# Performance work log

Hardware: AMD Instinct MI355X
Metric: run time of the kernel (lower is better)

Reference implementation:

```python
import jax, jax.numpy as jnp
import numpy as np

N_NODES = 100000
HIDDEN = 128
N_EDGES = 640000


def setup_inputs() -> dict:
    key = jax.random.key(0)
    k1, k2, k3, k4 = jax.random.split(key, 4)
    z_state = jax.random.normal(k1, (N_NODES, HIDDEN), dtype=jnp.float32)
    edge_label_index = jax.random.randint(k2, (2, N_EDGES), 0, N_NODES, dtype=jnp.int64)
    # Kaiming-ish init scale for the two linear layers (torch default ~ U(-1/sqrt(fan_in), ...))
    w1 = jax.random.normal(k3, (2 * HIDDEN, HIDDEN), dtype=jnp.float32) * (1.0 / np.sqrt(2 * HIDDEN))
    b1 = jnp.zeros((HIDDEN,), dtype=jnp.float32)
    w2 = jax.random.normal(k4, (HIDDEN, 1), dtype=jnp.float32) * (1.0 / np.sqrt(HIDDEN))
    b2 = jnp.zeros((1,), dtype=jnp.float32)
    return {
        "z_state": z_state,
        "edge_label_index": edge_label_index,
        "w1": w1,
        "b1": b1,
        "w2": w2,
        "b2": b2,
    }


def reference(z_state, edge_label_index, w1, b1, w2, b2):
    # Gather source/destination node embeddings: [E, H] each.
    src = z_state[edge_label_index[0]]
    dst = z_state[edge_label_index[1]]
    # Concatenate along features -> [E, 2H], then 2-layer MLP.
    z = jnp.concatenate([src, dst], axis=-1)
    h = jax.nn.relu(z @ w1 + b1)            # [E, H]
    out = jax.nn.sigmoid(h @ w2 + b2)        # [E, 1]
    return out.reshape(-1)
```

## Files before the change

### kernel.cpp

```cpp
#include <hip/hip_runtime.h>
#include <cstdint>
#include <cstddef>

#define HD 128
#define KD 256
#define NBMAX 512
#define SLOT 2560

typedef __attribute__((ext_vector_type(8))) short bf16x8;
typedef __attribute__((ext_vector_type(4))) float f32x4;
typedef __attribute__((ext_vector_type(4))) unsigned int u32x4;
typedef __attribute__((ext_vector_type(2))) _Float16 h16x2;
typedef __attribute__((ext_vector_type(4))) _Float16 h16x4;

typedef const __attribute__((address_space(1))) void gv_t;
typedef __attribute__((address_space(3))) void lv_t;

__device__ __forceinline__ void gload16(const void* g, void* l) {
    __builtin_amdgcn_global_load_lds((gv_t*)g, (lv_t*)l, 16, 0, 0);
}

__device__ __forceinline__ unsigned short f2bf(float x) {
    unsigned u = __float_as_uint(x);
    u = (u + 0x7fffu + ((u >> 16) & 1u)) >> 16;
    return (unsigned short)u;
}

__global__ void pack_zero_kernel(const float* __restrict__ w1,
                                 unsigned short* __restrict__ Bp,
                                 int* __restrict__ cursor) {
    if (blockIdx.x == 16) {
        if (cursor) { cursor[threadIdx.x] = 0; cursor[threadIdx.x + 256] = 0; }
        return;
    }
    const int tid = blockIdx.x * 256 + threadIdx.x;
    const int lane = tid & 63, nf = (tid >> 6) & 15, kt = tid >> 10;
    const int col = nf * 16 + (lane & 15);
    const int k0 = kt * 32 + (lane >> 4) * 8;
    #pragma unroll
    for (int j = 0; j < 8; ++j) {
        const int k = k0 + j;
        const float v = (col < HD) ? w1[(size_t)k * HD + col]
                                   : w1[(size_t)(HD + k) * HD + (col - HD)];
        Bp[(size_t)tid * 8 + j] = f2bf(v);
    }
}

__global__ void scatter_slot_kernel(const int* __restrict__ eli, const int E,
                                    int* __restrict__ cursor,
                                    int2* __restrict__ sorted) {
    __shared__ int lh[NBMAX];
    __shared__ int lb[NBMAX];
    const int t = threadIdx.x;
    const int nb = NBMAX;
    for (int b = t; b < nb; b += 256) lh[b] = 0;
    __syncthreads();
    const int per = (E + gridDim.x - 1) / gridDim.x;
    const int e0 = blockIdx.x * per;
    int e1 = e0 + per; if (e1 > E) e1 = E;
    for (int e = e0 + t; e < e1; e += 256)
        atomicAdd(&lh[eli[e] >> 8], 1);
    __syncthreads();
    for (int b = t; b < nb; b += 256) {
        const int c = lh[b];
        lb[b] = c ? atomicAdd(&cursor[b], c) : 0;
        lh[b] = 0;
    }
    __syncthreads();
    for (int e = e0 + t; e < e1; e += 256) {
        const int s = eli[e];
        const int b = s >> 8;
        const int r = atomicAdd(&lh[b], 1);
        const int idx = lb[b] + r;
        if (idx < SLOT)
            sorted[(size_t)b * SLOT + idx] = make_int2(eli[E + e], ((s & 255) << 20) | e);
    }
}

__global__ __launch_bounds__(256, 2) void uv_gemm_kernel(
    const float* __restrict__ z, const unsigned short* __restrict__ Bp,
    const float* __restrict__ b1, _Float16* __restrict__ UV, const int NN)
{
    __shared__ __attribute__((aligned(16))) unsigned short sA[64 * HD];
    __shared__ __attribute__((aligned(16))) unsigned short sB[32 * 1024];
    char* sAb = (char*)sA;
    const char* sBb = (const char*)sB;
    const int t = threadIdx.x, wave = t >> 6, l = t & 63;

    #pragma unroll
    for (int q = 0; q < 16; ++q) {
        const int i = wave * 16 + q;
        gload16((const char*)Bp + i * 1024 + l * 16, (char*)sB + i * 1024);
    }

    const int waveM = wave >> 1, waveN = wave & 1;
    const int ntiles = (NN + 63) >> 6;

    float4 bv[8];
    #pragma unroll
    for (int nf = 0; nf < 8; ++nf) {
        bv[nf] = make_float4(0.f, 0.f, 0.f, 0.f);
        if (waveN == 0) bv[nf] = *(const float4*)(b1 + nf * 16 + (l >> 4) * 4);
    }

    const int r = t >> 2, q4 = t & 3;

    for (int tile = blockIdx.x; tile < ntiles; tile += gridDim.x) {
        const int n0 = tile * 64;
        {
            int n = n0 + r; if (n >= NN) n = NN - 1;
            const float* zr = z + (size_t)n * HD + q4 * 32;
            #pragma unroll
            for (int q = 0; q < 8; ++q) {
                const float4 v = *(const float4*)(zr + q * 4);
                ushort4 o;
                o.x = f2bf(v.x); o.y = f2bf(v.y); o.z = f2bf(v.z); o.w = f2bf(v.w);
                const int byte = r * 256 + (q4 * 32 + q * 4) * 2;
                *(ushort4*)(sAb + (byte ^ ((r & 15) << 4))) = o;
            }
        }
        __syncthreads();

        f32x4 acc[2][8];
        #pragma unroll
        for (int nf = 0; nf < 8; ++nf)
            #pragma unroll
            for (int mf = 0; mf < 2; ++mf) {
                acc[mf][nf][0] = bv[nf].x; acc[mf][nf][1] = bv[nf].y;
                acc[mf][nf][2] = bv[nf].z; acc[mf][nf][3] = bv[nf].w;
            }
        #pragma unroll
        for (int kt = 0; kt < 4; ++kt) {
            bf16x8 bfr[8], af[2];
            #pragma unroll
            for (int nf = 0; nf < 8; ++nf)
                bfr[nf] = *(const bf16x8*)(sBb + (size_t)((kt * 16 + waveN * 8 + nf) * 64 + l) * 16);
            #pragma unroll
            for (int mf = 0; mf < 2; ++mf) {
                const int rr = waveM * 32 + mf * 16 + (l & 15);
                const int byte = rr * 256 + kt * 64 + (l >> 4) * 16;
                af[mf] = *(const bf16x8*)(sAb + (byte ^ ((rr & 15) << 4)));
            }
            #pragma unroll
            for (int mf = 0; mf < 2; ++mf)
                #pragma unroll
                for (int nf = 0; nf < 8; ++nf)
                    acc[mf][nf] = __builtin_amdgcn_mfma_f32_16x16x32_bf16(
                        bfr[nf], af[mf], acc[mf][nf], 0, 0, 0);
        }
        #pragma unroll
        for (int mf = 0; mf < 2; ++mf) {
            const int n2 = n0 + waveM * 32 + mf * 16 + (l & 15);
            if (n2 < NN) {
                #pragma unroll
                for (int nf = 0; nf < 8; ++nf) {
                    const int c0 = waveN * 128 + nf * 16 + (l >> 4) * 4;
                    h16x4 o = (h16x4){(_Float16)acc[mf][nf][0], (_Float16)acc[mf][nf][1],
                                      (_Float16)acc[mf][nf][2], (_Float16)acc[mf][nf][3]};
                    *(h16x4*)(UV + (size_t)n2 * KD + c0) = o;
                }
            }
        }
        __syncthreads();
    }
}

__global__ __launch_bounds__(256, 8) void edge_slot_kernel(
    const _Float16* __restrict__ UV, const int2* __restrict__ sorted,
    const int* __restrict__ cursor, const int NB,
    const float* __restrict__ w2, const float* __restrict__ b2,
    float* __restrict__ out)
{
    const int t = threadIdx.x, cl = t & 15, g = t >> 4;
    const int xcd = blockIdx.x & 7, rank = blockIdx.x >> 3;
    const int bpx = (NB + 7) >> 3;
    const int blo = xcd * bpx;
    if (blo >= NB) return;
    const int bhi = (blo + bpx < NB) ? (blo + bpx) : NB;
    const int nbk = bhi - blo;
    const int j = rank % nbk, sub = rank / nbk;
    const int nsub = (255 - j) / nbk + 1;
    const int b = blo + j;
    int cnt = cursor[b]; if (cnt > SLOT) cnt = SLOT;
    const size_t base = (size_t)b * SLOT;
    const int group = sub * 16 + g;
    const int stride = nsub * 16;

    h16x2 w2h[4];
    {
        const float4 wlo = *(const float4*)(w2 + cl * 8);
        const float4 whi = *(const float4*)(w2 + cl * 8 + 4);
        w2h[0] = (h16x2){(_Float16)wlo.x, (_Float16)wlo.y};
        w2h[1] = (h16x2){(_Float16)wlo.z, (_Float16)wlo.w};
        w2h[2] = (h16x2){(_Float16)whi.x, (_Float16)whi.y};
        w2h[3] = (h16x2){(_Float16)whi.z, (_Float16)whi.w};
    }
    const float bb2 = b2[0];
    const h16x2 zero2 = (h16x2){(_Float16)0.f, (_Float16)0.f};

    int i = group;
    if (i >= cnt) return;
    int2 q = sorted[base + i];
    int e = q.y & 0xFFFFF;
    int s = (b << 8) | ((q.y >> 20) & 255);
    u32x4 u = *(const u32x4*)(UV + (size_t)s * KD + cl * 8);
    u32x4 v = *(const u32x4*)(UV + (size_t)q.x * KD + HD + cl * 8);

    for (;;) {
        const int i2 = i + stride;
        int e2 = 0; u32x4 un, vn;
        if (i2 < cnt) {
            const int2 q2 = sorted[base + i2];
            e2 = q2.y & 0xFFFFF;
            const int s2 = (b << 8) | ((q2.y >> 20) & 255);
            un = *(const u32x4*)(UV + (size_t)s2 * KD + cl * 8);
            vn = *(const u32x4*)(UV + (size_t)q2.x * KD + HD + cl * 8);
        }
        h16x2 acc2 = zero2;
        #pragma unroll
        for (int m = 0; m < 4; ++m) {
            union { unsigned int ui; h16x2 h2; } cu, cv;
            cu.ui = u[m]; cv.ui = v[m];
            const h16x2 h = __builtin_elementwise_max(cu.h2 + cv.h2, zero2);
            acc2 = acc2 + h * w2h[m];
        }
        float acc = (float)acc2[0] + (float)acc2[1];
        #pragma unroll
        for (int msk = 1; msk <= 8; msk <<= 1) acc += __shfl_xor(acc, msk);
        if (cl == 0) out[e] = 1.f / (1.f + __expf(-(acc + bb2)));
        if (i2 >= cnt) break;
        i = i2; e = e2; u = un; v = vn;
    }
}


__global__ __launch_bounds__(256, 8) void edge_uv_f16_kernel(
    const _Float16* __restrict__ UV, const int* __restrict__ eli,
    const int E, const float* __restrict__ w2, const float* __restrict__ b2,
    float* __restrict__ out)
{
    const int t = threadIdx.x;
    const int cl = t & 15;
    const int gid = (blockIdx.x * 256 + t) >> 4;
    const int ng = (gridDim.x * 256) >> 4;

    h16x2 w2h[4];
    {
        const float4 wlo = *(const float4*)(w2 + cl * 8);
        const float4 whi = *(const float4*)(w2 + cl * 8 + 4);
        w2h[0] = (h16x2){(_Float16)wlo.x, (_Float16)wlo.y};
        w2h[1] = (h16x2){(_Float16)wlo.z, (_Float16)wlo.w};
        w2h[2] = (h16x2){(_Float16)whi.x, (_Float16)whi.y};
        w2h[3] = (h16x2){(_Float16)whi.z, (_Float16)whi.w};
    }
    const float bb2 = b2[0];
    const h16x2 zero2 = (h16x2){(_Float16)0.f, (_Float16)0.f};

    int e = gid;
    if (e >= E) return;
    int s = eli[e], d = eli[E + e];
    u32x4 u = *(const u32x4*)(UV + (size_t)s * KD + cl * 8);
    u32x4 v = *(const u32x4*)(UV + (size_t)d * KD + HD + cl * 8);
    int en = e + ng;
    int enc = (en < E) ? en : (E - 1);
    int sn = eli[enc], dn = eli[E + enc];

    for (;;) {
        const int e2 = en + ng;
        const int e2c = (e2 < E) ? e2 : (E - 1);
        const int s2 = eli[e2c], d2 = eli[E + e2c];
        const u32x4 un = *(const u32x4*)(UV + (size_t)sn * KD + cl * 8);
        const u32x4 vn = *(const u32x4*)(UV + (size_t)dn * KD + HD + cl * 8);

        h16x2 acc2 = zero2;
        #pragma unroll
        for (int m = 0; m < 4; ++m) {
            union { unsigned int ui; h16x2 h2; } cu, cv;
            cu.ui = u[m]; cv.ui = v[m];
            const h16x2 h = __builtin_elementwise_max(cu.h2 + cv.h2, zero2);
            acc2 = acc2 + h * w2h[m];
        }
        float acc = (float)acc2[0] + (float)acc2[1];
        #pragma unroll
        for (int msk = 1; msk <= 8; msk <<= 1) acc += __shfl_xor(acc, msk);
        if (cl == 0) out[e] = 1.f / (1.f + __expf(-(acc + bb2)));

        if (en >= E) break;
        e = en; u = un; v = vn;
        en = e2; sn = s2; dn = d2;
    }
}


__global__ __launch_bounds__(256, 2) void edge_decoder_fp32_kernel(
    const float* __restrict__ z, const int* __restrict__ eli, const int E,
    const float* __restrict__ w1, const float* __restrict__ b1,
    const float* __restrict__ w2, const float* __restrict__ b2,
    float* __restrict__ out)
{
    __shared__ float sZ[32][256];
    __shared__ float sW[2][32][128];
    const int t = threadIdx.x, wave = t >> 6, lane = t & 63;
    const int e0 = blockIdx.x * 32;
    #pragma unroll
    for (int q = 0; q < 8; ++q) {
        const int e = wave * 8 + q;
        int ge = e0 + e; if (ge >= E) ge = E - 1;
        const int node = (lane < 32) ? eli[ge] : eli[E + ge];
        gload16(z + (size_t)node * HD + (size_t)(lane & 31) * 4, &sZ[e][0]);
    }
    #pragma unroll
    for (int q = 0; q < 4; ++q) {
        const int inst = wave * 4 + q;
        gload16(w1 + inst * 256 + lane * 4, &sW[0][0][0] + inst * 256);
    }
    __syncthreads();
    const int cg = t & 31, eg = t >> 5, c0 = cg * 4;
    float acc[4][4] = {{0.f,0.f,0.f,0.f}};
    for (int kc = 0; kc < 8; ++kc) {
        const int buf = kc & 1;
        if (kc + 1 < 8) {
            const float* gw = w1 + (size_t)(kc + 1) * 32 * HD;
            #pragma unroll
            for (int q = 0; q < 4; ++q) {
                const int inst = wave * 4 + q;
                gload16(gw + inst * 256 + lane * 4, &sW[buf ^ 1][0][0] + inst * 256);
            }
        }
        #pragma unroll
        for (int k4 = 0; k4 < 8; ++k4) {
            float zr[4][4];
            #pragma unroll
            for (int i = 0; i < 4; ++i)
                *(float4*)(&zr[i][0]) = *(const float4*)(&sZ[eg*4+i][kc*32 + k4*4]);
            #pragma unroll
            for (int kk = 0; kk < 4; ++kk) {
                const float4 wv = *(const float4*)(&sW[buf][k4*4+kk][c0]);
                #pragma unroll
                for (int i = 0; i < 4; ++i) {
                    acc[i][0] = fmaf(zr[i][kk], wv.x, acc[i][0]);
                    acc[i][1] = fmaf(zr[i][kk], wv.y, acc[i][1]);
                    acc[i][2] = fmaf(zr[i][kk], wv.z, acc[i][2]);
                    acc[i][3] = fmaf(zr[i][kk], wv.w, acc[i][3]);
                }
            }
        }
        __syncthreads();
    }
    const float4 b1v = *(const float4*)(&b1[c0]);
    const float4 w2v = *(const float4*)(&w2[c0]);
    const float bb2 = b2[0];
    float part[4];
    #pragma unroll
    for (int i = 0; i < 4; ++i)
        part[i] = fmaxf(acc[i][0]+b1v.x,0.f)*w2v.x + fmaxf(acc[i][1]+b1v.y,0.f)*w2v.y
                + fmaxf(acc[i][2]+b1v.z,0.f)*w2v.z + fmaxf(acc[i][3]+b1v.w,0.f)*w2v.w;
    #pragma unroll
    for (int m = 16; m >= 1; m >>= 1)
        #pragma unroll
        for (int i = 0; i < 4; ++i) part[i] += __shfl_xor(part[i], m, 32);
    if (cg == 0) {
        #pragma unroll
        for (int i = 0; i < 4; ++i) {
            const int ge = e0 + eg * 4 + i;
            if (ge < E) out[ge] = 1.0f / (1.0f + __expf(-(part[i] + bb2)));
        }
    }
}

extern "C" void kernel_launch(void* const* d_in, const int* in_sizes, int n_in,
                              void* d_out, int out_size, void* d_ws, size_t ws_size,
                              hipStream_t stream) {
    const float* z  = (const float*)d_in[0];
    const int* eli  = (const int*)d_in[1];
    const float* w1 = (const float*)d_in[2];
    const float* b1 = (const float*)d_in[3];
    const float* w2 = (const float*)d_in[4];
    const float* b2 = (const float*)d_in[5];
    float* out = (float*)d_out;

    const int E  = in_sizes[1] / 2;
    const int NN = in_sizes[0] / HD;
    const int NB = (NN + 255) >> 8;

    size_t off = 0;
    auto take = [&](size_t n) { size_t r = off; off = (off + n + 15) & ~(size_t)15; return r; };
    const size_t o_uv    = take((size_t)NN * KD * 2);
    const size_t o_bp    = take(65536);
    const size_t need_uv = off;
    const size_t o_cur   = take(NBMAX * 4);
    const size_t o_sort  = take((size_t)NB * SLOT * 8);
    const size_t need_sorted = off;

    if (ws_size >= need_sorted && NB <= NBMAX && E < (1 << 20)) {
        _Float16* UV = (_Float16*)((char*)d_ws + o_uv);
        unsigned short* Bp = (unsigned short*)((char*)d_ws + o_bp);
        int* cursor  = (int*)((char*)d_ws + o_cur);
        int2* sorted = (int2*)((char*)d_ws + o_sort);

        pack_zero_kernel<<<17, 256, 0, stream>>>(w1, Bp, cursor);
        scatter_slot_kernel<<<256, 256, 0, stream>>>(eli, E, cursor, sorted);
        uv_gemm_kernel<<<512, 256, 0, stream>>>(z, Bp, b1, UV, NN);
        edge_slot_kernel<<<2048, 256, 0, stream>>>(UV, sorted, cursor, NB, w2, b2, out);
    } else if (ws_size >= need_uv) {
        _Float16* UV = (_Float16*)((char*)d_ws + o_uv);
        unsigned short* Bp = (unsigned short*)((char*)d_ws + o_bp);
        pack_zero_kernel<<<16, 256, 0, stream>>>(w1, Bp, (int*)nullptr);
        uv_gemm_kernel<<<512, 256, 0, stream>>>(z, Bp, b1, UV, NN);
        edge_uv_f16_kernel<<<2048, 256, 0, stream>>>(UV, eli, E, w2, b2, out);
    } else {
        edge_decoder_fp32_kernel<<<(E + 31) / 32, 256, 0, stream>>>(
            z, eli, E, w1, b1, w2, b2, out);
    }
}
```

Baseline: 93.81 us.

## Keep W1 fragments in registers and load A directly from global in UV GEMM

The UV GEMM kernel stops staging W1 and the z tile through LDS. Each wave now holds all its W1 bf16 fragments in registers for the whole kernel and loads its A fragments straight from global memory, converting them to bf16 in registers. This removes both __syncthreads per tile and the LDS round trips, but raises register pressure (32 bf16x8 B fragments per thread) and uses less coalesced global reads for z. The scatter kernel launch is also raised from 256 to 512 blocks.

```diff
diff --git a/kernel.cpp b/kernel.cpp
--- a/kernel.cpp
+++ b/kernel.cpp
@@ -81,20 +81,16 @@
     const float* __restrict__ z, const unsigned short* __restrict__ Bp,
     const float* __restrict__ b1, _Float16* __restrict__ UV, const int NN)
 {
-    __shared__ __attribute__((aligned(16))) unsigned short sA[64 * HD];
-    __shared__ __attribute__((aligned(16))) unsigned short sB[32 * 1024];
-    char* sAb = (char*)sA;
-    const char* sBb = (const char*)sB;
     const int t = threadIdx.x, wave = t >> 6, l = t & 63;
-
-    #pragma unroll
-    for (int q = 0; q < 16; ++q) {
-        const int i = wave * 16 + q;
-        gload16((const char*)Bp + i * 1024 + l * 16, (char*)sB + i * 1024);
-    }
-
     const int waveM = wave >> 1, waveN = wave & 1;
     const int ntiles = (NN + 63) >> 6;
+
+    bf16x8 bfr[4][8];
+    #pragma unroll
+    for (int kt = 0; kt < 4; ++kt)
+        #pragma unroll
+        for (int nf = 0; nf < 8; ++nf)
+            bfr[kt][nf] = *(const bf16x8*)(Bp + (size_t)((kt * 16 + waveN * 8 + nf) * 64 + l) * 8);
 
     float4 bv[8];
     #pragma unroll
@@ -103,24 +99,10 @@
         if (waveN == 0) bv[nf] = *(const float4*)(b1 + nf * 16 + (l >> 4) * 4);
     }
 
-    const int r = t >> 2, q4 = t & 3;
+    const int colsel = (l >> 4) * 8;
 
     for (int tile = blockIdx.x; tile < ntiles; tile += gridDim.x) {
         const int n0 = tile * 64;
-        {
-            int n = n0 + r; if (n >= NN) n = NN - 1;
-            const float* zr = z + (size_t)n * HD + q4 * 32;
-            #pragma unroll
-            for (int q = 0; q < 8; ++q) {
-                const float4 v = *(const float4*)(zr + q * 4);
-                ushort4 o;
-                o.x = f2bf(v.x); o.y = f2bf(v.y); o.z = f2bf(v.z); o.w = f2bf(v.w);
-                const int byte = r * 256 + (q4 * 32 + q * 4) * 2;
-                *(ushort4*)(sAb + (byte ^ ((r & 15) << 4))) = o;
-            }
-        }
-        __syncthreads();
-
         f32x4 acc[2][8];
         #pragma unroll
         for (int nf = 0; nf < 8; ++nf)
@@ -130,23 +112,28 @@
                 acc[mf][nf][2] = bv[nf].z; acc[mf][nf][3] = bv[nf].w;
             }
         #pragma unroll
-        for (int kt = 0; kt < 4; ++kt) {
-            bf16x8 bfr[8], af[2];
-            #pragma unroll
-            for (int nf = 0; nf < 8; ++nf)
-                bfr[nf] = *(const bf16x8*)(sBb + (size_t)((kt * 16 + waveN * 8 + nf) * 64 + l) * 16);
-            #pragma unroll
-            for (int mf = 0; mf < 2; ++mf) {
-                const int rr = waveM * 32 + mf * 16 + (l & 15);
-                const int byte = rr * 256 + kt * 64 + (l >> 4) * 16;
-                af[mf] = *(const bf16x8*)(sAb + (byte ^ ((rr & 15) << 4)));
+        for (int mf = 0; mf < 2; ++mf) {
+            int r = n0 + waveM * 32 + mf * 16 + (l & 15);
+            if (r >= NN) r = NN - 1;
+            const float* zr = z + (size_t)r * HD;
+            bf16x8 af[4];
+            #pragma unroll
+            for (int kt = 0; kt < 4; ++kt) {
+                const float4 a = *(const float4*)(zr + kt * 32 + colsel);
+                const float4 b = *(const float4*)(zr + kt * 32 + colsel + 4);
+                bf16x8 f;
+                f[0] = (short)f2bf(a.x); f[1] = (short)f2bf(a.y);
+                f[2] = (short)f2bf(a.z); f[3] = (short)f2bf(a.w);
+                f[4] = (short)f2bf(b.x); f[5] = (short)f2bf(b.y);
+                f[6] = (short)f2bf(b.z); f[7] = (short)f2bf(b.w);
+                af[kt] = f;
             }
             #pragma unroll
-            for (int mf = 0; mf < 2; ++mf)
+            for (int kt = 0; kt < 4; ++kt)
                 #pragma unroll
                 for (int nf = 0; nf < 8; ++nf)
                     acc[mf][nf] = __builtin_amdgcn_mfma_f32_16x16x32_bf16(
-                        bfr[nf], af[mf], acc[mf][nf], 0, 0, 0);
+                        bfr[kt][nf], af[kt], acc[mf][nf], 0, 0, 0);
         }
         #pragma unroll
         for (int mf = 0; mf < 2; ++mf) {
@@ -161,7 +148,6 @@
                 }
             }
         }
-        __syncthreads();
     }
 }
 
@@ -399,7 +385,7 @@
         int2* sorted = (int2*)((char*)d_ws + o_sort);
 
         pack_zero_kernel<<<17, 256, 0, stream>>>(w1, Bp, cursor);
-        scatter_slot_kernel<<<256, 256, 0, stream>>>(eli, E, cursor, sorted);
+        scatter_slot_kernel<<<512, 256, 0, stream>>>(eli, E, cursor, sorted);
         uv_gemm_kernel<<<512, 256, 0, stream>>>(z, Bp, b1, UV, NN);
         edge_slot_kernel<<<2048, 256, 0, stream>>>(UV, sorted, cursor, NB, w2, b2, out);
     } else if (ws_size >= need_uv) {
```

New measurement: 96.89 us. 1.03x slower.
